# Kernel tuning notes

Hardware: AMD Instinct MI355X
Metric: run time of the kernel (lower is better)

Reference implementation:

```python
import jax, jax.numpy as jnp
import numpy as np


def setup_inputs() -> dict:
    key = jax.random.key(0)
    k1, k2, k3 = jax.random.split(key, 3)
    N, E, C = 100000, 3200000, 256
    x = jax.random.normal(k1, (N, C), dtype=jnp.float32)
    edge_index = jax.random.randint(k2, (2, E), 0, N, dtype=jnp.int64)
    W = jax.random.normal(k3, (C, 1), dtype=jnp.float32) / np.sqrt(C)
    b = jnp.zeros((1,), dtype=jnp.float32)
    return {"x": x, "edge_index": edge_index, "W": W, "b": b}


def reference(x, edge_index, W, b):
    # GCNConv(in_channels, 1) with default add_self_loops=True, symmetric norm,
    # followed by Softplus.
    N = x.shape[0]
    loop = jnp.arange(N, dtype=edge_index.dtype)
    src = jnp.concatenate([edge_index[0], loop])  # [E+N]
    dst = jnp.concatenate([edge_index[1], loop])  # [E+N]
    # degree on target index (unit edge weights, self-loops included)
    deg = jax.ops.segment_sum(jnp.ones_like(dst, dtype=x.dtype), dst, num_segments=N)
    dinv = jnp.where(deg > 0, jax.lax.rsqrt(deg), 0.0)
    norm = dinv[src] * dinv[dst]  # [E+N]
    h = x @ W  # [N, 1] linear transform before aggregation (no bias)
    msg = norm[:, None] * h[src]  # [E+N, 1]
    out = jax.ops.segment_sum(msg, dst, num_segments=N) + b  # [N, 1]
    return jax.nn.softplus(out)
```

## Files before the change

kernel.cpp:

```cpp
#include <hip/hip_runtime.h>
#include <cmath>
#include <cstdint>


#define NBSHIFT 8
#define NLOCAL  (1 << NBSHIFT)
#define KPART   1024
#define SRCBITS 17

__global__ __launch_bounds__(256) void k_front(const float* __restrict__ x,
                                               const float* __restrict__ W,
                                               const int* __restrict__ dst,
                                               float* __restrict__ h,
                                               unsigned* __restrict__ countsT,
                                               int N, int E, int NB, int CH) {
    int tid  = blockIdx.x * blockDim.x + threadIdx.x;
    int lane = threadIdx.x & 63;
    int nw   = (gridDim.x * blockDim.x) >> 6;
    const float4 wv = *reinterpret_cast<const float4*>(W + lane * 4);
    for (int row = tid >> 6; row < N; row += nw) {
        const float4 xv = *reinterpret_cast<const float4*>(x + (size_t)row * 256 + lane * 4);
        float s = xv.x * wv.x + xv.y * wv.y + xv.z * wv.z + xv.w * wv.w;
        #pragma unroll
        for (int o = 32; o >= 1; o >>= 1) s += __shfl_xor(s, o, 64);
        if (lane == 0) h[row] = s;
    }

    __shared__ unsigned cnt[512];
    for (int j = threadIdx.x; j < 512; j += 256) cnt[j] = 0;
    __syncthreads();
    int s = blockIdx.x * CH, e = min(E, s + CH);
    int e4 = s + (((e - s) >> 2) << 2);
    for (int i = s + (int)threadIdx.x * 4; i < e4; i += 1024) {
        int4 v = *reinterpret_cast<const int4*>(dst + i);
        atomicAdd(&cnt[((unsigned)v.x) >> NBSHIFT], 1u);
        atomicAdd(&cnt[((unsigned)v.y) >> NBSHIFT], 1u);
        atomicAdd(&cnt[((unsigned)v.z) >> NBSHIFT], 1u);
        atomicAdd(&cnt[((unsigned)v.w) >> NBSHIFT], 1u);
    }
    for (int i = e4 + threadIdx.x; i < e; i += 256)
        atomicAdd(&cnt[((unsigned)dst[i]) >> NBSHIFT], 1u);
    __syncthreads();
    for (int j = threadIdx.x; j < NB; j += 256)
        countsT[(size_t)j * KPART + blockIdx.x] = cnt[j];
}

__global__ __launch_bounds__(256) void k_scanA(const unsigned* __restrict__ countsT,
                                               unsigned* __restrict__ btot) {
    __shared__ unsigned red[256];
    int j = blockIdx.x, t = threadIdx.x;
    uint4 c = *reinterpret_cast<const uint4*>(countsT + (size_t)j * KPART + t * 4);
    red[t] = c.x + c.y + c.z + c.w;
    __syncthreads();
    for (int s = 128; s > 0; s >>= 1) {
        if (t < s) red[t] += red[t + s];
        __syncthreads();
    }
    if (t == 0) btot[j] = red[0];
}

__global__ __launch_bounds__(256) void k_scanC(const unsigned* __restrict__ countsT,
                                               const unsigned* __restrict__ btot,
                                               unsigned* __restrict__ bbase,
                                               unsigned* __restrict__ baseT,
                                               int NB) {
    __shared__ unsigned red[256];
    __shared__ unsigned arr[256];
    __shared__ unsigned sBase;
    int j = blockIdx.x, t = threadIdx.x;

    unsigned v = 0;
    if (t < j) v += btot[t];
    if (t + 256 < j) v += btot[t + 256];
    red[t] = v;
    __syncthreads();
    for (int s = 128; s > 0; s >>= 1) {
        if (t < s) red[t] += red[t + s];
        __syncthreads();
    }
    if (t == 0) { sBase = red[0]; bbase[j] = red[0]; }

    uint4 c = *reinterpret_cast<const uint4*>(countsT + (size_t)j * KPART + t * 4);
    unsigned own = c.x + c.y + c.z + c.w;
    arr[t] = own;
    __syncthreads();
    for (int off = 1; off < 256; off <<= 1) {
        unsigned add = (t >= off) ? arr[t - off] : 0u;
        __syncthreads();
        arr[t] += add;
        __syncthreads();
    }
    unsigned base = sBase + (arr[t] - own);
    uint4 o;
    o.x = base;
    o.y = base + c.x;
    o.z = base + c.x + c.y;
    o.w = base + c.x + c.y + c.z;
    *reinterpret_cast<uint4*>(baseT + (size_t)j * KPART + t * 4) = o;
}

__global__ __launch_bounds__(256) void k_part(const int* __restrict__ src,
                                              const int* __restrict__ dst,
                                              const unsigned* __restrict__ baseT,
                                              unsigned* __restrict__ sorted,
                                              int E, int NB, int CH) {
    __shared__ unsigned base[512];
    __shared__ unsigned rank[512];
    for (int j = threadIdx.x; j < NB; j += 256) {
        base[j] = baseT[(size_t)j * KPART + blockIdx.x];
        rank[j] = 0;
    }
    __syncthreads();
    int s = blockIdx.x * CH, e = min(E, s + CH);
    int e4 = s + (((e - s) >> 2) << 2);
    for (int i = s + (int)threadIdx.x * 4; i < e4; i += 1024) {
        int4 dv = *reinterpret_cast<const int4*>(dst + i);
        int4 sv = *reinterpret_cast<const int4*>(src + i);
        unsigned d, j, r;
        d = (unsigned)dv.x; j = d >> NBSHIFT; r = atomicAdd(&rank[j], 1u);
        sorted[base[j] + r] = ((d & (NLOCAL - 1u)) << SRCBITS) | (unsigned)sv.x;
        d = (unsigned)dv.y; j = d >> NBSHIFT; r = atomicAdd(&rank[j], 1u);
        sorted[base[j] + r] = ((d & (NLOCAL - 1u)) << SRCBITS) | (unsigned)sv.y;
        d = (unsigned)dv.z; j = d >> NBSHIFT; r = atomicAdd(&rank[j], 1u);
        sorted[base[j] + r] = ((d & (NLOCAL - 1u)) << SRCBITS) | (unsigned)sv.z;
        d = (unsigned)dv.w; j = d >> NBSHIFT; r = atomicAdd(&rank[j], 1u);
        sorted[base[j] + r] = ((d & (NLOCAL - 1u)) << SRCBITS) | (unsigned)sv.w;
    }
    for (int i = e4 + threadIdx.x; i < e; i += 256) {
        unsigned d = (unsigned)dst[i];
        unsigned j = d >> NBSHIFT;
        unsigned r = atomicAdd(&rank[j], 1u);
        sorted[base[j] + r] = ((d & (NLOCAL - 1u)) << SRCBITS) | (unsigned)src[i];
    }
}

__global__ __launch_bounds__(1024) void k_deg(const unsigned* __restrict__ sorted,
                                              const unsigned* __restrict__ bbase,
                                              const unsigned* __restrict__ btot,
                                              const float* __restrict__ h,
                                              float* __restrict__ dinv,
                                              float* __restrict__ g,
                                              int N) {
    __shared__ unsigned acc[NLOCAL];
    int j = blockIdx.x, t = threadIdx.x;
    if (t < NLOCAL) acc[t] = 0;
    __syncthreads();
    unsigned s0 = bbase[j], e0 = s0 + btot[j];
    for (unsigned i = s0 + t; i < e0; i += 1024)
        atomicAdd(&acc[sorted[i] >> SRCBITS], 1u);
    __syncthreads();
    if (t < NLOCAL) {
        int n = (j << NBSHIFT) + t;
        if (n < N) {
            float di = rsqrtf((float)(acc[t] + 1u));
            dinv[n] = di;
            g[n]    = di * h[n];
        }
    }
}

__global__ __launch_bounds__(1024) void k_agg(const unsigned* __restrict__ sorted,
                                              const unsigned* __restrict__ bbase,
                                              const unsigned* __restrict__ btot,
                                              const float* __restrict__ g,
                                              const float* __restrict__ dinv,
                                              const float* __restrict__ b,
                                              float* __restrict__ out,
                                              int N) {
    __shared__ float acc[NLOCAL];
    int j = blockIdx.x, t = threadIdx.x;
    if (t < NLOCAL) acc[t] = 0.0f;
    __syncthreads();
    unsigned s0 = bbase[j], e0 = s0 + btot[j];
    for (unsigned i = s0 + t; i < e0; i += 1024) {
        unsigned p = sorted[i];
        atomicAdd(&acc[p >> SRCBITS], g[p & ((1u << SRCBITS) - 1u)]);
    }
    __syncthreads();
    if (t < NLOCAL) {
        int n = (j << NBSHIFT) + t;
        if (n < N) {
            float v = dinv[n] * (acc[t] + g[n]) + b[0];
            out[n] = fmaxf(v, 0.0f) + log1pf(expf(-fabsf(v)));
        }
    }
}

extern "C" void kernel_launch(void* const* d_in, const int* in_sizes, int n_in,
                              void* d_out, int out_size, void* d_ws, size_t ws_size,
                              hipStream_t stream) {
    const float* x  = (const float*)d_in[0];
    const int*   ei = (const int*)d_in[1];
    const float* W  = (const float*)d_in[2];
    const float* b  = (const float*)d_in[3];
    float* out = (float*)d_out;

    int N = in_sizes[0] / 256;
    int E = in_sizes[1] / 2;
    const int* src = ei;
    const int* dst = ei + E;

    int NB = (N + NLOCAL - 1) >> NBSHIFT;
    int CH = (((E + KPART - 1) / KPART) + 3) & ~3;

    float*    h       = (float*)d_ws;
    float*    dinv    = h + N;
    float*    g       = dinv + N;
    unsigned* sorted  = (unsigned*)(g + N);
    unsigned* countsT = sorted + E;
    unsigned* baseT   = countsT + (size_t)NB * KPART;
    unsigned* btot    = baseT + (size_t)NB * KPART;
    unsigned* bbase   = btot + NB;

    k_front<<<KPART, 256, 0, stream>>>(x, W, dst, h, countsT, N, E, NB, CH);
    k_scanA<<<NB, 256, 0, stream>>>(countsT, btot);
    k_scanC<<<NB, 256, 0, stream>>>(countsT, btot, bbase, baseT, NB);
    k_part <<<KPART, 256, 0, stream>>>(src, dst, baseT, sorted, E, NB, CH);
    k_deg  <<<NB, 1024, 0, stream>>>(sorted, bbase, btot, h, dinv, g, N);
    k_agg  <<<NB, 1024, 0, stream>>>(sorted, bbase, btot, g, dinv, b, out, N);
}
```

Before: 238.3 us.

## Merge scan kernels via decoupled publish flags and halve destination bucket size

Merges the two bucket-scan kernels into one. Each block publishes its bucket total to a flagged 64-bit slot and spin-waits on lower buckets' flags, which removes one launch. Buckets shrink from 256 to 128 nodes, doubling their number to about 782 so the aggregation kernels run more, smaller blocks of 512 threads. The counting loop now reads 8 destinations per iteration. The risks are a spin-wait deadlock if lower buckets are not co-resident or scheduled first, and more countsT/baseT traffic from having more buckets.

```diff
diff --git a/kernel.cpp b/kernel.cpp
--- a/kernel.cpp
+++ b/kernel.cpp
@@ -3,85 +3,102 @@
 #include <cstdint>
 
 
-#define NBSHIFT 8
+#define NBSHIFT 7
 #define NLOCAL  (1 << NBSHIFT)
-#define KPART   1024
+#define NBLK    1024
 #define SRCBITS 17
+#define PUBFLAG (1ULL << 63)
 
 __global__ __launch_bounds__(256) void k_front(const float* __restrict__ x,
                                                const float* __restrict__ W,
                                                const int* __restrict__ dst,
                                                float* __restrict__ h,
                                                unsigned* __restrict__ countsT,
+                                               unsigned long long* __restrict__ pub,
                                                int N, int E, int NB, int CH) {
-    int tid  = blockIdx.x * blockDim.x + threadIdx.x;
-    int lane = threadIdx.x & 63;
-    int nw   = (gridDim.x * blockDim.x) >> 6;
-    const float4 wv = *reinterpret_cast<const float4*>(W + lane * 4);
-    for (int row = tid >> 6; row < N; row += nw) {
-        const float4 xv = *reinterpret_cast<const float4*>(x + (size_t)row * 256 + lane * 4);
-        float s = xv.x * wv.x + xv.y * wv.y + xv.z * wv.z + xv.w * wv.w;
-        #pragma unroll
-        for (int o = 32; o >= 1; o >>= 1) s += __shfl_xor(s, o, 64);
-        if (lane == 0) h[row] = s;
-    }
-
-    __shared__ unsigned cnt[512];
-    for (int j = threadIdx.x; j < 512; j += 256) cnt[j] = 0;
-    __syncthreads();
-    int s = blockIdx.x * CH, e = min(E, s + CH);
-    int e4 = s + (((e - s) >> 2) << 2);
-    for (int i = s + (int)threadIdx.x * 4; i < e4; i += 1024) {
-        int4 v = *reinterpret_cast<const int4*>(dst + i);
-        atomicAdd(&cnt[((unsigned)v.x) >> NBSHIFT], 1u);
-        atomicAdd(&cnt[((unsigned)v.y) >> NBSHIFT], 1u);
-        atomicAdd(&cnt[((unsigned)v.z) >> NBSHIFT], 1u);
-        atomicAdd(&cnt[((unsigned)v.w) >> NBSHIFT], 1u);
-    }
-    for (int i = e4 + threadIdx.x; i < e; i += 256)
+    const int t = threadIdx.x, blk = blockIdx.x;
+
+    if (blk == 0)
+        for (int j = t; j < NB; j += 256) pub[j] = 0ULL;
+
+    {
+        int lane = t & 63;
+        int nw   = (NBLK * 256) >> 6;
+        const float4 wv = *reinterpret_cast<const float4*>(W + lane * 4);
+        for (int row = (blk * 256 + t) >> 6; row < N; row += nw) {
+            const float4 xv = *reinterpret_cast<const float4*>(x + (size_t)row * 256 + lane * 4);
+            float s = xv.x * wv.x + xv.y * wv.y + xv.z * wv.z + xv.w * wv.w;
+            #pragma unroll
+            for (int o = 32; o >= 1; o >>= 1) s += __shfl_xor(s, o, 64);
+            if (lane == 0) h[row] = s;
+        }
+    }
+
+    __shared__ unsigned cnt[1024];
+    for (int j = t; j < 1024; j += 256) cnt[j] = 0;
+    __syncthreads();
+    int cs = blk * CH, ce = min(E, cs + CH);
+    int e8 = cs + (((ce - cs) >> 3) << 3);
+    for (int i = cs + t * 8; i < e8; i += 2048) {
+        int4 a = *reinterpret_cast<const int4*>(dst + i);
+        int4 c = *reinterpret_cast<const int4*>(dst + i + 4);
+        atomicAdd(&cnt[((unsigned)a.x) >> NBSHIFT], 1u);
+        atomicAdd(&cnt[((unsigned)a.y) >> NBSHIFT], 1u);
+        atomicAdd(&cnt[((unsigned)a.z) >> NBSHIFT], 1u);
+        atomicAdd(&cnt[((unsigned)a.w) >> NBSHIFT], 1u);
+        atomicAdd(&cnt[((unsigned)c.x) >> NBSHIFT], 1u);
+        atomicAdd(&cnt[((unsigned)c.y) >> NBSHIFT], 1u);
+        atomicAdd(&cnt[((unsigned)c.z) >> NBSHIFT], 1u);
+        atomicAdd(&cnt[((unsigned)c.w) >> NBSHIFT], 1u);
+    }
+    for (int i = e8 + t; i < ce; i += 256)
         atomicAdd(&cnt[((unsigned)dst[i]) >> NBSHIFT], 1u);
     __syncthreads();
-    for (int j = threadIdx.x; j < NB; j += 256)
-        countsT[(size_t)j * KPART + blockIdx.x] = cnt[j];
-}
-
-__global__ __launch_bounds__(256) void k_scanA(const unsigned* __restrict__ countsT,
-                                               unsigned* __restrict__ btot) {
-    __shared__ unsigned red[256];
-    int j = blockIdx.x, t = threadIdx.x;
-    uint4 c = *reinterpret_cast<const uint4*>(countsT + (size_t)j * KPART + t * 4);
-    red[t] = c.x + c.y + c.z + c.w;
-    __syncthreads();
-    for (int s = 128; s > 0; s >>= 1) {
-        if (t < s) red[t] += red[t + s];
-        __syncthreads();
-    }
-    if (t == 0) btot[j] = red[0];
-}
-
-__global__ __launch_bounds__(256) void k_scanC(const unsigned* __restrict__ countsT,
-                                               const unsigned* __restrict__ btot,
-                                               unsigned* __restrict__ bbase,
-                                               unsigned* __restrict__ baseT,
-                                               int NB) {
+    for (int j = t; j < NB; j += 256)
+        countsT[(size_t)j * NBLK + blk] = cnt[j];
+}
+
+__global__ __launch_bounds__(256) void k_scan(const unsigned* __restrict__ countsT,
+                                              unsigned long long* __restrict__ pub,
+                                              unsigned* __restrict__ btot,
+                                              unsigned* __restrict__ bbase,
+                                              unsigned* __restrict__ baseT,
+                                              int NB) {
     __shared__ unsigned red[256];
     __shared__ unsigned arr[256];
     __shared__ unsigned sBase;
     int j = blockIdx.x, t = threadIdx.x;
 
-    unsigned v = 0;
-    if (t < j) v += btot[t];
-    if (t + 256 < j) v += btot[t + 256];
-    red[t] = v;
+    uint4 c = *reinterpret_cast<const uint4*>(countsT + (size_t)j * NBLK + t * 4);
+    unsigned own = c.x + c.y + c.z + c.w;
+    red[t] = own;
     __syncthreads();
     for (int s = 128; s > 0; s >>= 1) {
         if (t < s) red[t] += red[t + s];
         __syncthreads();
     }
+    unsigned total = red[0];
+    if (t == 0) {
+        btot[j] = total;
+        atomicExch(&pub[j], PUBFLAG | (unsigned long long)total);
+    }
+
+    unsigned v = 0;
+    for (int k = t; k < j; k += 256) {
+        unsigned long long p;
+        while (!((p = atomicAdd(&pub[k], 0ULL)) & PUBFLAG))
+            __builtin_amdgcn_s_sleep(2);
+        v += (unsigned)p;
+    }
+    __syncthreads();
+    red[t] = v;
+    __syncthreads();
+    for (int s = 128; s > 0; s >>= 1) {
+        if (t < s) red[t] += red[t + s];
+        __syncthreads();
+    }
     if (t == 0) { sBase = red[0]; bbase[j] = red[0]; }
 
-    uint4 c = *reinterpret_cast<const uint4*>(countsT + (size_t)j * KPART + t * 4);
-    unsigned own = c.x + c.y + c.z + c.w;
     arr[t] = own;
     __syncthreads();
     for (int off = 1; off < 256; off <<= 1) {
@@ -96,7 +113,7 @@
     o.y = base + c.x;
     o.z = base + c.x + c.y;
     o.w = base + c.x + c.y + c.z;
-    *reinterpret_cast<uint4*>(baseT + (size_t)j * KPART + t * 4) = o;
+    *reinterpret_cast<uint4*>(baseT + (size_t)j * NBLK + t * 4) = o;
 }
 
 __global__ __launch_bounds__(256) void k_part(const int* __restrict__ src,
@@ -104,16 +121,15 @@
                                               const unsigned* __restrict__ baseT,
                                               unsigned* __restrict__ sorted,
                                               int E, int NB, int CH) {
-    __shared__ unsigned base[512];
-    __shared__ unsigned rank[512];
-    for (int j = threadIdx.x; j < NB; j += 256) {
-        base[j] = baseT[(size_t)j * KPART + blockIdx.x];
-        rank[j] = 0;
-    }
-    __syncthreads();
-    int s = blockIdx.x * CH, e = min(E, s + CH);
-    int e4 = s + (((e - s) >> 2) << 2);
-    for (int i = s + (int)threadIdx.x * 4; i < e4; i += 1024) {
+    __shared__ unsigned base[1024];
+    __shared__ unsigned rank[1024];
+    const int t = threadIdx.x, blk = blockIdx.x;
+    for (int j = t; j < 1024; j += 256) rank[j] = 0;
+    for (int j = t; j < NB; j += 256) base[j] = baseT[(size_t)j * NBLK + blk];
+    __syncthreads();
+    int cs = blk * CH, ce = min(E, cs + CH);
+    int e4 = cs + (((ce - cs) >> 2) << 2);
+    for (int i = cs + t * 4; i < e4; i += 1024) {
         int4 dv = *reinterpret_cast<const int4*>(dst + i);
         int4 sv = *reinterpret_cast<const int4*>(src + i);
         unsigned d, j, r;
@@ -126,7 +142,7 @@
         d = (unsigned)dv.w; j = d >> NBSHIFT; r = atomicAdd(&rank[j], 1u);
         sorted[base[j] + r] = ((d & (NLOCAL - 1u)) << SRCBITS) | (unsigned)sv.w;
     }
-    for (int i = e4 + threadIdx.x; i < e; i += 256) {
+    for (int i = e4 + t; i < ce; i += 256) {
         unsigned d = (unsigned)dst[i];
         unsigned j = d >> NBSHIFT;
         unsigned r = atomicAdd(&rank[j], 1u);
@@ -134,19 +150,19 @@
     }
 }
 
-__global__ __launch_bounds__(1024) void k_deg(const unsigned* __restrict__ sorted,
-                                              const unsigned* __restrict__ bbase,
-                                              const unsigned* __restrict__ btot,
-                                              const float* __restrict__ h,
-                                              float* __restrict__ dinv,
-                                              float* __restrict__ g,
-                                              int N) {
+__global__ __launch_bounds__(512) void k_deg(const unsigned* __restrict__ sorted,
+                                             const unsigned* __restrict__ bbase,
+                                             const unsigned* __restrict__ btot,
+                                             const float* __restrict__ h,
+                                             float* __restrict__ dinv,
+                                             float* __restrict__ g,
+                                             int N) {
     __shared__ unsigned acc[NLOCAL];
     int j = blockIdx.x, t = threadIdx.x;
     if (t < NLOCAL) acc[t] = 0;
     __syncthreads();
     unsigned s0 = bbase[j], e0 = s0 + btot[j];
-    for (unsigned i = s0 + t; i < e0; i += 1024)
+    for (unsigned i = s0 + t; i < e0; i += 512)
         atomicAdd(&acc[sorted[i] >> SRCBITS], 1u);
     __syncthreads();
     if (t < NLOCAL) {
@@ -159,20 +175,20 @@
     }
 }
 
-__global__ __launch_bounds__(1024) void k_agg(const unsigned* __restrict__ sorted,
-                                              const unsigned* __restrict__ bbase,
-                                              const unsigned* __restrict__ btot,
-                                              const float* __restrict__ g,
-                                              const float* __restrict__ dinv,
-                                              const float* __restrict__ b,
-                                              float* __restrict__ out,
-                                              int N) {
+__global__ __launch_bounds__(512) void k_agg(const unsigned* __restrict__ sorted,
+                                             const unsigned* __restrict__ bbase,
+                                             const unsigned* __restrict__ btot,
+                                             const float* __restrict__ g,
+                                             const float* __restrict__ dinv,
+                                             const float* __restrict__ b,
+                                             float* __restrict__ out,
+                                             int N) {
     __shared__ float acc[NLOCAL];
     int j = blockIdx.x, t = threadIdx.x;
     if (t < NLOCAL) acc[t] = 0.0f;
     __syncthreads();
     unsigned s0 = bbase[j], e0 = s0 + btot[j];
-    for (unsigned i = s0 + t; i < e0; i += 1024) {
+    for (unsigned i = s0 + t; i < e0; i += 512) {
         unsigned p = sorted[i];
         atomicAdd(&acc[p >> SRCBITS], g[p & ((1u << SRCBITS) - 1u)]);
     }
@@ -201,21 +217,22 @@
     const int* dst = ei + E;
 
     int NB = (N + NLOCAL - 1) >> NBSHIFT;
-    int CH = (((E + KPART - 1) / KPART) + 3) & ~3;
+    int CH = (((E + NBLK - 1) / NBLK) + 7) & ~7;
 
     float*    h       = (float*)d_ws;
     float*    dinv    = h + N;
     float*    g       = dinv + N;
     unsigned* sorted  = (unsigned*)(g + N);
     unsigned* countsT = sorted + E;
-    unsigned* baseT   = countsT + (size_t)NB * KPART;
-    unsigned* btot    = baseT + (size_t)NB * KPART;
+    unsigned* baseT   = countsT + (size_t)NB * NBLK;
+    unsigned* btot    = baseT + (size_t)NB * NBLK;
     unsigned* bbase   = btot + NB;
-
-    k_front<<<KPART, 256, 0, stream>>>(x, W, dst, h, countsT, N, E, NB, CH);
-    k_scanA<<<NB, 256, 0, stream>>>(countsT, btot);
-    k_scanC<<<NB, 256, 0, stream>>>(countsT, btot, bbase, baseT, NB);
-    k_part <<<KPART, 256, 0, stream>>>(src, dst, baseT, sorted, E, NB, CH);
-    k_deg  <<<NB, 1024, 0, stream>>>(sorted, bbase, btot, h, dinv, g, N);
-    k_agg  <<<NB, 1024, 0, stream>>>(sorted, bbase, btot, g, dinv, b, out, N);
-}
+    uintptr_t pa = (uintptr_t)(bbase + NB);
+    unsigned long long* pub = (unsigned long long*)((pa + 7) & ~(uintptr_t)7);
+
+    k_front<<<NBLK, 256, 0, stream>>>(x, W, dst, h, countsT, pub, N, E, NB, CH);
+    k_scan <<<NB, 256, 0, stream>>>(countsT, pub, btot, bbase, baseT, NB);
+    k_part <<<NBLK, 256, 0, stream>>>(src, dst, baseT, sorted, E, NB, CH);
+    k_deg  <<<NB, 512, 0, stream>>>(sorted, bbase, btot, h, dinv, g, N);
+    k_agg  <<<NB, 512, 0, stream>>>(sorted, bbase, btot, g, dinv, b, out, N);
+}
```

Measured after the change: 257.8 us. +8.2%, slower.
